# Optimization experiments

Measured on AMD Instinct MI355X. Metric: run time of the kernel, lower is better.

Reference implementation:

```python
import jax, jax.numpy as jnp
import numpy as np

N = 200000      # n_edges (1-simplices)
NNZ = 2000000   # nonzeros per sparse Laplacian
F_IN = 64       # num_edge_feats
F_H = 32        # f_size (hard-coded in FlowSAN)
F_OUT = 8       # output_size
G = 256         # number of graphs in batch
NEG_SLOPE = 0.2 # GAT LeakyReLU slope


def setup_inputs() -> dict:
    key = jax.random.key(0)
    ks = iter(jax.random.split(key, 64))

    def rn(shape, s=0.1):
        return jax.random.normal(next(ks), shape, dtype=jnp.float32) * s

    d = {"x1": jax.random.normal(next(ks), (N, F_IN), dtype=jnp.float32)}
    dims = [(F_IN, F_H), (F_H, F_H), (F_H, F_H), (F_H, F_OUT)]
    for i, (fi, fo) in enumerate(dims, 1):
        d[f"pW{i}"] = rn((fi, fo))                      # SANLayer.p_layer weight (bias=False)
        d[f"uW{i}"] = rn((fi, fo))                      # l_u GAT linear
        d[f"ua_s{i}"] = rn((fo,)); d[f"ua_d{i}"] = rn((fo,))  # l_u GAT attention vec halves
        d[f"dW{i}"] = rn((fi, fo))                      # l_d GAT linear
        d[f"da_s{i}"] = rn((fo,)); d[f"da_d{i}"] = rn((fo,))
    d["l1_idx"] = jax.random.randint(next(ks), (2, NNZ), 0, N, dtype=jnp.int32)
    d["l1_val"] = jax.random.normal(next(ks), (NNZ,), dtype=jnp.float32)
    d["lu_idx"] = jax.random.randint(next(ks), (2, NNZ), 0, N, dtype=jnp.int32)
    d["ld_idx"] = jax.random.randint(next(ks), (2, NNZ), 0, N, dtype=jnp.int32)
    d["batch1"] = jnp.sort(jax.random.randint(next(ks), (N,), 0, G, dtype=jnp.int32))
    return d


def _gat(x, W, a_s, a_d, idx):
    # GAT-style attention over the nonzero pattern of the sparse Laplacian
    h = x @ W                                   # [N, fo]
    row, col = idx[0], idx[1]
    e = jax.nn.leaky_relu(h[row] @ a_s + h[col] @ a_d, NEG_SLOPE)  # [nnz]
    e = e - jax.ops.segment_max(e, row, num_segments=N)[row]       # stable softmax
    w = jnp.exp(e)
    alpha = w / (jax.ops.segment_sum(w, row, num_segments=N)[row] + 1e-16)
    return jax.ops.segment_sum(alpha[:, None] * h[col], row, num_segments=N)


def _san(x, pW, uW, ua_s, ua_d, dW, da_s, da_d, l1_idx, l1_val, lu_idx, ld_idx):
    # p branch: torch.sparse.mm(L1, x @ pW)
    hp = x @ pW
    row, col = l1_idx[0], l1_idx[1]
    hp = jax.ops.segment_sum(l1_val[:, None] * hp[col], row, num_segments=N)
    hu = _gat(x, uW, ua_s, ua_d, lu_idx)
    hd = _gat(x, dW, da_s, da_d, ld_idx)
    return hu + hd + hp


def reference(x1,
              pW1, uW1, ua_s1, ua_d1, dW1, da_s1, da_d1,
              pW2, uW2, ua_s2, ua_d2, dW2, da_s2, da_d2,
              pW3, uW3, ua_s3, ua_d3, dW3, da_s3, da_d3,
              pW4, uW4, ua_s4, ua_d4, dW4, da_s4, da_d4,
              l1_idx, l1_val, lu_idx, ld_idx, batch1):
    layers = [
        (pW1, uW1, ua_s1, ua_d1, dW1, da_s1, da_d1),
        (pW2, uW2, ua_s2, ua_d2, dW2, da_s2, da_d2),
        (pW3, uW3, ua_s3, ua_d3, dW3, da_s3, da_d3),
        (pW4, uW4, ua_s4, ua_d4, dW4, da_s4, da_d4),
    ]
    x = x1
    for p in layers:
        x = jax.nn.relu(_san(x, *p, l1_idx, l1_val, lu_idx, ld_idx))
    # global_mean_pool(|x|, batch1)
    cnt = jax.ops.segment_sum(jnp.ones((N,), jnp.float32), batch1, num_segments=G)
    pooled = jax.ops.segment_sum(jnp.abs(x), batch1, num_segments=G) / jnp.maximum(cnt, 1.0)[:, None]
    return jax.nn.softmax(pooled, axis=1)
```

## Files before the change

### kernel.cpp

```cpp
#include <hip/hip_runtime.h>
#include <hip/hip_fp16.h>
#include <cmath>


#define N_    200000
#define NNZ_  2000000
#define G_    256


__global__ __launch_bounds__(256) void hist_k(const int* __restrict__ lu, const int* __restrict__ ld,
                                              const int* __restrict__ l1, int* __restrict__ deg,
                                              int* __restrict__ tick) {
    int i = blockIdx.x * 256 + threadIdx.x;
    if (i >= NNZ_ / 4) return;
    int e = i * 4;
    int4 ru = *reinterpret_cast<const int4*>(lu + e);
    int4 rd = *reinterpret_cast<const int4*>(ld + e);
    int4 rl = *reinterpret_cast<const int4*>(l1 + e);
    int4 t;
    t.x = atomicAdd(&deg[ru.x], 1);
    t.y = atomicAdd(&deg[ru.y], 1);
    t.z = atomicAdd(&deg[ru.z], 1);
    t.w = atomicAdd(&deg[ru.w], 1);
    *reinterpret_cast<int4*>(tick + e) = t;
    t.x = atomicAdd(&deg[N_ + rd.x], 1);
    t.y = atomicAdd(&deg[N_ + rd.y], 1);
    t.z = atomicAdd(&deg[N_ + rd.z], 1);
    t.w = atomicAdd(&deg[N_ + rd.w], 1);
    *reinterpret_cast<int4*>(tick + NNZ_ + e) = t;
    t.x = atomicAdd(&deg[2 * N_ + rl.x], 1);
    t.y = atomicAdd(&deg[2 * N_ + rl.y], 1);
    t.z = atomicAdd(&deg[2 * N_ + rl.z], 1);
    t.w = atomicAdd(&deg[2 * N_ + rl.w], 1);
    *reinterpret_cast<int4*>(tick + 2 * NNZ_ + e) = t;
}

__global__ __launch_bounds__(256) void scan1_k(const int* __restrict__ in, int* __restrict__ out,
                                               int* __restrict__ bsum, int n) {
    __shared__ int lds[256];
    int tid = threadIdx.x;
    int base = blockIdx.x * 1024 + tid * 4;
    int v0 = (base + 0 < n) ? in[base + 0] : 0;
    int v1 = (base + 1 < n) ? in[base + 1] : 0;
    int v2 = (base + 2 < n) ? in[base + 2] : 0;
    int v3 = (base + 3 < n) ? in[base + 3] : 0;
    int s = v0 + v1 + v2 + v3;
    lds[tid] = s;
    __syncthreads();
    for (int off = 1; off < 256; off <<= 1) {
        int t = (tid >= off) ? lds[tid - off] : 0;
        __syncthreads();
        lds[tid] += t;
        __syncthreads();
    }
    int excl = lds[tid] - s;
    if (base + 0 < n) out[base + 0] = excl;
    if (base + 1 < n) out[base + 1] = excl + v0;
    if (base + 2 < n) out[base + 2] = excl + v0 + v1;
    if (base + 3 < n) out[base + 3] = excl + v0 + v1 + v2;
    if (tid == 255) bsum[blockIdx.x] = lds[255];
}

__global__ __launch_bounds__(256) void scan2_k(int* __restrict__ bsum, int nb, int* __restrict__ total_out) {
    __shared__ int lds[256];
    __shared__ int run_s;
    int tid = threadIdx.x;
    if (tid == 0) run_s = 0;
    __syncthreads();
    for (int c0 = 0; c0 < nb; c0 += 256) {
        int i = c0 + tid;
        int s = (i < nb) ? bsum[i] : 0;
        lds[tid] = s;
        __syncthreads();
        for (int off = 1; off < 256; off <<= 1) {
            int t = (tid >= off) ? lds[tid - off] : 0;
            __syncthreads();
            lds[tid] += t;
            __syncthreads();
        }
        int run = run_s;
        if (i < nb) bsum[i] = run + lds[tid] - s;
        __syncthreads();
        if (tid == 0) run_s = run + lds[255];
        __syncthreads();
    }
    if (tid == 0 && total_out) *total_out = run_s;
}

__global__ __launch_bounds__(256) void scan3_k(int* __restrict__ out, const int* __restrict__ bsum, int n) {
    int add = bsum[blockIdx.x];
    int base = blockIdx.x * 1024 + threadIdx.x * 4;
    #pragma unroll
    for (int k = 0; k < 4; ++k)
        if (base + k < n) out[base + k] += add;
}


template <int FI, int FO, int SCB>
__global__ __launch_bounds__(256) void scat_gemm_k(
    const int* __restrict__ lu, const int* __restrict__ ld, const int* __restrict__ l1,
    const float* __restrict__ l1v, const int* __restrict__ rptr, const int* __restrict__ tick,
    int* __restrict__ cols_u, int* __restrict__ cols_d, int2* __restrict__ pl,
    const float* __restrict__ x,
    const float* __restrict__ uW, const float* __restrict__ uas, const float* __restrict__ uad,
    const float* __restrict__ dW, const float* __restrict__ das, const float* __restrict__ dad,
    const float* __restrict__ pW,
    __half* __restrict__ HU, __half* __restrict__ HD, __half* __restrict__ HP,
    float* __restrict__ ssu, float* __restrict__ sdu,
    float* __restrict__ ssd, float* __restrict__ sdd) {
    if (blockIdx.x % 13 == 0) {
        int sid = blockIdx.x / 13;
        if (sid >= SCB) return;
        int i = sid * 256 + threadIdx.x;
        if (i >= NNZ_ / 4) return;
        int e = i * 4;
        int4 ru = *reinterpret_cast<const int4*>(lu + e);
        int4 rd = *reinterpret_cast<const int4*>(ld + e);
        int4 rl = *reinterpret_cast<const int4*>(l1 + e);
        int4 cu = *reinterpret_cast<const int4*>(lu + NNZ_ + e);
        int4 cd = *reinterpret_cast<const int4*>(ld + NNZ_ + e);
        int4 cl = *reinterpret_cast<const int4*>(l1 + NNZ_ + e);
        int4 tu = *reinterpret_cast<const int4*>(tick + e);
        int4 td = *reinterpret_cast<const int4*>(tick + NNZ_ + e);
        int4 tl = *reinterpret_cast<const int4*>(tick + 2 * NNZ_ + e);
        float4 v = *reinterpret_cast<const float4*>(l1v + e);
        int pu0 = rptr[ru.x] + tu.x, pu1 = rptr[ru.y] + tu.y;
        int pu2 = rptr[ru.z] + tu.z, pu3 = rptr[ru.w] + tu.w;
        int pd0 = rptr[N_ + rd.x] + td.x - NNZ_, pd1 = rptr[N_ + rd.y] + td.y - NNZ_;
        int pd2 = rptr[N_ + rd.z] + td.z - NNZ_, pd3 = rptr[N_ + rd.w] + td.w - NNZ_;
        int pl0 = rptr[2 * N_ + rl.x] + tl.x - 2 * NNZ_, pl1 = rptr[2 * N_ + rl.y] + tl.y - 2 * NNZ_;
        int pl2 = rptr[2 * N_ + rl.z] + tl.z - 2 * NNZ_, pl3 = rptr[2 * N_ + rl.w] + tl.w - 2 * NNZ_;
        __builtin_nontemporal_store(cu.x, &cols_u[pu0]);
        __builtin_nontemporal_store(cu.y, &cols_u[pu1]);
        __builtin_nontemporal_store(cu.z, &cols_u[pu2]);
        __builtin_nontemporal_store(cu.w, &cols_u[pu3]);
        __builtin_nontemporal_store(cd.x, &cols_d[pd0]);
        __builtin_nontemporal_store(cd.y, &cols_d[pd1]);
        __builtin_nontemporal_store(cd.z, &cols_d[pd2]);
        __builtin_nontemporal_store(cd.w, &cols_d[pd3]);
        long long q0 = ((long long)__float_as_int(v.x) << 32) | (unsigned)cl.x;
        long long q1 = ((long long)__float_as_int(v.y) << 32) | (unsigned)cl.y;
        long long q2 = ((long long)__float_as_int(v.z) << 32) | (unsigned)cl.z;
        long long q3 = ((long long)__float_as_int(v.w) << 32) | (unsigned)cl.w;
        __builtin_nontemporal_store(q0, (long long*)&pl[pl0]);
        __builtin_nontemporal_store(q1, (long long*)&pl[pl1]);
        __builtin_nontemporal_store(q2, (long long*)&pl[pl2]);
        __builtin_nontemporal_store(q3, (long long*)&pl[pl3]);
        return;
    }
    int gid = blockIdx.x - blockIdx.x / 13 - 1;
    constexpr int ROWS = 256 / FO;
    constexpr int XS = FI + 1;
    __shared__ float Wu[FI * FO], Wd[FI * FO], Wp[FI * FO];
    __shared__ float xs[ROWS * XS];
    int tid = threadIdx.x;
    for (int i = tid; i < FI * FO; i += 256) {
        Wu[i] = uW[i];
        Wd[i] = dW[i];
        Wp[i] = pW[i];
    }
    int row0 = gid * ROWS;
    for (int i = tid; i < ROWS * FI; i += 256) {
        int r = i / FI, k = i - r * FI;
        int gr = row0 + r;
        xs[r * XS + k] = (gr < N_) ? x[(size_t)gr * FI + k] : 0.f;
    }
    __syncthreads();
    int r = tid / FO, j = tid - (tid / FO) * FO;
    int grow = row0 + r;
    float au = 0.f, ad = 0.f, ap = 0.f;
    #pragma unroll
    for (int k = 0; k < FI; ++k) {
        float xv = xs[r * XS + k];
        au = fmaf(xv, Wu[k * FO + j], au);
        ad = fmaf(xv, Wd[k * FO + j], ad);
        ap = fmaf(xv, Wp[k * FO + j], ap);
    }
    if (grow < N_) {
        HU[(size_t)grow * FO + j] = __float2half(au);
        HD[(size_t)grow * FO + j] = __float2half(ad);
        HP[(size_t)grow * FO + j] = __float2half(ap);
    }
    float vsu = au * uas[j], vdu = au * uad[j];
    float vsd = ad * das[j], vdd = ad * dad[j];
    #pragma unroll
    for (int m = FO / 2; m >= 1; m >>= 1) {
        vsu += __shfl_xor(vsu, m, FO);
        vdu += __shfl_xor(vdu, m, FO);
        vsd += __shfl_xor(vsd, m, FO);
        vdd += __shfl_xor(vdd, m, FO);
    }
    if (j == 0 && grow < N_) {
        ssu[grow] = vsu; sdu[grow] = vdu;
        ssd[grow] = vsd; sdd[grow] = vdd;
    }
}


template <int FI, int FO>
__global__ __launch_bounds__(256) void gemm3_k(const float* __restrict__ x,
                                               const float* __restrict__ uW, const float* __restrict__ uas,
                                               const float* __restrict__ uad,
                                               const float* __restrict__ dW, const float* __restrict__ das,
                                               const float* __restrict__ dad,
                                               const float* __restrict__ pW,
                                               __half* __restrict__ HU, __half* __restrict__ HD,
                                               __half* __restrict__ HP,
                                               float* __restrict__ ssu, float* __restrict__ sdu,
                                               float* __restrict__ ssd, float* __restrict__ sdd) {
    constexpr int ROWS = 256 / FO;
    constexpr int XS = FI + 1;
    __shared__ float Wu[FI * FO], Wd[FI * FO], Wp[FI * FO];
    __shared__ float xs[ROWS * XS];
    int tid = threadIdx.x;
    for (int i = tid; i < FI * FO; i += 256) {
        Wu[i] = uW[i];
        Wd[i] = dW[i];
        Wp[i] = pW[i];
    }
    int row0 = blockIdx.x * ROWS;
    for (int i = tid; i < ROWS * FI; i += 256) {
        int r = i / FI, k = i - r * FI;
        int gr = row0 + r;
        xs[r * XS + k] = (gr < N_) ? x[(size_t)gr * FI + k] : 0.f;
    }
    __syncthreads();
    int r = tid / FO, j = tid - (tid / FO) * FO;
    int grow = row0 + r;
    float au = 0.f, ad = 0.f, ap = 0.f;
    #pragma unroll
    for (int k = 0; k < FI; ++k) {
        float xv = xs[r * XS + k];
        au = fmaf(xv, Wu[k * FO + j], au);
        ad = fmaf(xv, Wd[k * FO + j], ad);
        ap = fmaf(xv, Wp[k * FO + j], ap);
    }
    if (grow < N_) {
        HU[(size_t)grow * FO + j] = __float2half(au);
        HD[(size_t)grow * FO + j] = __float2half(ad);
        HP[(size_t)grow * FO + j] = __float2half(ap);
    }
    float vsu = au * uas[j], vdu = au * uad[j];
    float vsd = ad * das[j], vdd = ad * dad[j];
    #pragma unroll
    for (int m = FO / 2; m >= 1; m >>= 1) {
        vsu += __shfl_xor(vsu, m, FO);
        vdu += __shfl_xor(vdu, m, FO);
        vsd += __shfl_xor(vsd, m, FO);
        vdd += __shfl_xor(vdd, m, FO);
    }
    if (j == 0 && grow < N_) {
        ssu[grow] = vsu; sdu[grow] = vdu;
        ssd[grow] = vsd; sdd[grow] = vdd;
    }
}


template <int FO>
__global__ __launch_bounds__(256) void gather3_k(const int* __restrict__ rptr,
                                                 const int* __restrict__ cols_u,
                                                 const int* __restrict__ cols_d,
                                                 const int2* __restrict__ pl,
                                                 const __half* __restrict__ HU,
                                                 const __half* __restrict__ HD,
                                                 const __half* __restrict__ HP,
                                                 const float* __restrict__ ssu, const float* __restrict__ sdu,
                                                 const float* __restrict__ ssd, const float* __restrict__ sdd,
                                                 float* __restrict__ xout) {
    constexpr int LPR = FO / 8;
    constexpr int SLOTS = 64 / LPR;
    int lane = threadIdx.x & 63;
    int wv = threadIdx.x >> 6;
    int fs = lane & (LPR - 1);
    int slot = lane / LPR;
    int r = blockIdx.x * 4 + wv;
    if (r >= N_) return;

    float out[8];
    #pragma unroll
    for (int k = 0; k < 8; ++k) out[k] = 0.f;

    #pragma unroll
    for (int br = 0; br < 2; ++br) {
        const int* cols = br == 0 ? cols_u : cols_d;
        const __half* H = br == 0 ? HU : HD;
        const float* sdv = br == 0 ? sdu : sdd;
        const float* ssv = br == 0 ? ssu : ssd;
        int base = br == 0 ? 0 : N_;
        int boff = br == 0 ? 0 : NNZ_;
        int b = rptr[base + r] - boff, e = rptr[base + r + 1] - boff;
        float s_row = ssv[r];
        float acc[8];
        #pragma unroll
        for (int k = 0; k < 8; ++k) acc[k] = 0.f;
        float z = 0.f;
        for (int p0 = b; p0 < e; p0 += SLOTS) {
            int p = p0 + slot;
            bool valid = p < e;
            int pc = valid ? p : e - 1;
            int c = cols[pc];
            float g = s_row + sdv[c];
            g = g > 0.f ? g : 0.2f * g;
            float w = valid ? __expf(g) : 0.f;
            z += w;
            const float4 hv = *reinterpret_cast<const float4*>(H + (size_t)c * FO + fs * 8);
            const __half2* h2 = reinterpret_cast<const __half2*>(&hv);
            #pragma unroll
            for (int k = 0; k < 4; ++k) {
                float2 f = __half22float2(h2[k]);
                acc[2 * k]     = fmaf(w, f.x, acc[2 * k]);
                acc[2 * k + 1] = fmaf(w, f.y, acc[2 * k + 1]);
            }
        }
        #pragma unroll
        for (int m = LPR; m < 64; m <<= 1) z += __shfl_xor(z, m);
        float inv = 1.f / (z + 1e-16f);
        #pragma unroll
        for (int k = 0; k < 8; ++k) out[k] = fmaf(acc[k], inv, out[k]);
    }

    {
        int b = rptr[2 * N_ + r] - 2 * NNZ_, e = rptr[2 * N_ + r + 1] - 2 * NNZ_;
        for (int p0 = b; p0 < e; p0 += SLOTS) {
            int p = p0 + slot;
            bool valid = p < e;
            int pc = valid ? p : e - 1;
            int2 cv = pl[pc];
            int c = cv.x;
            float w = valid ? __int_as_float(cv.y) : 0.f;
            const float4 hv = *reinterpret_cast<const float4*>(HP + (size_t)c * FO + fs * 8);
            const __half2* h2 = reinterpret_cast<const __half2*>(&hv);
            #pragma unroll
            for (int k = 0; k < 4; ++k) {
                float2 f = __half22float2(h2[k]);
                out[2 * k]     = fmaf(w, f.x, out[2 * k]);
                out[2 * k + 1] = fmaf(w, f.y, out[2 * k + 1]);
            }
        }
    }

    #pragma unroll
    for (int k = 0; k < 8; ++k) {
        #pragma unroll
        for (int m = LPR; m < 64; m <<= 1) out[k] += __shfl_xor(out[k], m);
    }
    if (slot == 0) {
        float4 o0 = make_float4(fmaxf(out[0], 0.f), fmaxf(out[1], 0.f),
                                fmaxf(out[2], 0.f), fmaxf(out[3], 0.f));
        float4 o1 = make_float4(fmaxf(out[4], 0.f), fmaxf(out[5], 0.f),
                                fmaxf(out[6], 0.f), fmaxf(out[7], 0.f));
        float* op = xout + (size_t)r * FO + fs * 8;
        *reinterpret_cast<float4*>(op) = o0;
        *reinterpret_cast<float4*>(op + 4) = o1;
    }
}


__global__ __launch_bounds__(256) void pool_k(const float* __restrict__ x, const int* __restrict__ batch,
                                              float* __restrict__ out) {
    int g = blockIdx.x;
    __shared__ float part[256];
    __shared__ int sse[2];
    if (threadIdx.x < 2) {
        int target = g + threadIdx.x;
        int lo = 0, hi = N_;
        while (lo < hi) {
            int mid = (lo + hi) >> 1;
            if (batch[mid] < target) lo = mid + 1; else hi = mid;
        }
        sse[threadIdx.x] = lo;
    }
    __syncthreads();
    int s = sse[0], e = sse[1];
    int f = threadIdx.x % 8;
    float acc = 0.f;
    for (int i = s + threadIdx.x / 8; i < e; i += 32) acc += fabsf(x[(size_t)i * 8 + f]);
    part[threadIdx.x] = acc;
    __syncthreads();
    if (threadIdx.x < 8) {
        float t = 0.f;
        #pragma unroll
        for (int k = 0; k < 32; ++k) t += part[k * 8 + f];
        float cnt = (float)(e - s);
        part[f] = t / fmaxf(cnt, 1.0f);
    }
    __syncthreads();
    if (threadIdx.x == 0) {
        float m = part[0];
        for (int j = 1; j < 8; ++j) m = fmaxf(m, part[j]);
        float zs = 0.f;
        float ex[8];
        for (int j = 0; j < 8; ++j) { ex[j] = __expf(part[j] - m); zs += ex[j]; }
        for (int j = 0; j < 8; ++j) out[g * 8 + j] = ex[j] / zs;
    }
}


template <int FI, int FO>
static void run_layer(const float* xin, float* xout, const float* const* W,
                      __half* HU, __half* HD, __half* HP,
                      float* SSU, float* SDU, float* SSD, float* SDD,
                      const int* PTR, const int* CU, const int* CD, const int2* PL,
                      hipStream_t stream) {
    constexpr int ROWS = 256 / FO;
    gemm3_k<FI, FO><<<(N_ + ROWS - 1) / ROWS, 256, 0, stream>>>(
        xin, W[1], W[2], W[3], W[4], W[5], W[6], W[0],
        HU, HD, HP, SSU, SDU, SSD, SDD);
    gather3_k<FO><<<(N_ + 3) / 4, 256, 0, stream>>>(
        PTR, CU, CD, PL, HU, HD, HP, SSU, SDU, SSD, SDD, xout);
}

extern "C" void kernel_launch(void* const* d_in, const int* in_sizes, int n_in, void* d_out,
                              int out_size, void* d_ws, size_t ws_size, hipStream_t stream) {
    (void)in_sizes; (void)n_in; (void)out_size; (void)ws_size;
    const float* x1     = (const float*)d_in[0];
    const int*   l1_idx = (const int*)d_in[29];
    const float* l1_val = (const float*)d_in[30];
    const int*   lu_idx = (const int*)d_in[31];
    const int*   ld_idx = (const int*)d_in[32];
    const int*   batch1 = (const int*)d_in[33];
    float* out = (float*)d_out;

    char* w = (char*)d_ws;
    size_t off = 0;
    auto alloc = [&](size_t bytes) -> char* {
        char* p = w + off;
        off = (off + bytes + 255) & ~(size_t)255;
        return p;
    };
    float*  X    = (float*)alloc((size_t)N_ * 32 * 4);
    __half* HU   = (__half*)alloc((size_t)N_ * 32 * 2);
    __half* HD   = (__half*)alloc((size_t)N_ * 32 * 2);
    __half* HP   = (__half*)alloc((size_t)N_ * 32 * 2);
    float*  SSU  = (float*)alloc((size_t)N_ * 4);
    float*  SDU  = (float*)alloc((size_t)N_ * 4);
    float*  SSD  = (float*)alloc((size_t)N_ * 4);
    float*  SDD  = (float*)alloc((size_t)N_ * 4);
    int*    PTR  = (int*)alloc((size_t)(3 * N_ + 1) * 4);
    int*    DEG  = (int*)alloc((size_t)3 * N_ * 4);
    int*    BSUM = (int*)alloc((size_t)1024 * 4);
    int*    TICK = (int*)alloc((size_t)3 * NNZ_ * 4);
    int*    CU   = (int*)alloc((size_t)NNZ_ * 4);
    int*    CD   = (int*)alloc((size_t)NNZ_ * 4);
    int2*   PL   = (int2*)alloc((size_t)NNZ_ * 8);

    const float* W0[7] = {(const float*)d_in[1], (const float*)d_in[2], (const float*)d_in[3],
                          (const float*)d_in[4], (const float*)d_in[5], (const float*)d_in[6],
                          (const float*)d_in[7]};
    const float* W1[7] = {(const float*)d_in[8],  (const float*)d_in[9],  (const float*)d_in[10],
                          (const float*)d_in[11], (const float*)d_in[12], (const float*)d_in[13],
                          (const float*)d_in[14]};
    const float* W2[7] = {(const float*)d_in[15], (const float*)d_in[16], (const float*)d_in[17],
                          (const float*)d_in[18], (const float*)d_in[19], (const float*)d_in[20],
                          (const float*)d_in[21]};
    const float* W3[7] = {(const float*)d_in[22], (const float*)d_in[23], (const float*)d_in[24],
                          (const float*)d_in[25], (const float*)d_in[26], (const float*)d_in[27],
                          (const float*)d_in[28]};

    hipMemsetAsync(DEG, 0, (size_t)3 * N_ * 4, stream);
    constexpr int QBL = (NNZ_ / 4 + 255) / 256;
    hist_k<<<QBL, 256, 0, stream>>>(lu_idx, ld_idx, l1_idx, DEG, TICK);
    int n3 = 3 * N_;
    int nb = (n3 + 1023) / 1024;
    scan1_k<<<nb, 256, 0, stream>>>(DEG, PTR, BSUM, n3);
    scan2_k<<<1, 256, 0, stream>>>(BSUM, nb, PTR + n3);
    scan3_k<<<nb, 256, 0, stream>>>(PTR, BSUM, n3);

    {
        constexpr int T = 27100;
        scat_gemm_k<64, 32, QBL><<<T, 256, 0, stream>>>(
            lu_idx, ld_idx, l1_idx, l1_val, PTR, TICK, CU, CD, PL,
            x1, W0[1], W0[2], W0[3], W0[4], W0[5], W0[6], W0[0],
            HU, HD, HP, SSU, SDU, SSD, SDD);
    }
    gather3_k<32><<<(N_ + 3) / 4, 256, 0, stream>>>(
        PTR, CU, CD, PL, HU, HD, HP, SSU, SDU, SSD, SDD, X);

    run_layer<32, 32>(X, X, W1, HU, HD, HP, SSU, SDU, SSD, SDD, PTR, CU, CD, PL, stream);
    run_layer<32, 32>(X, X, W2, HU, HD, HP, SSU, SDU, SSD, SDD, PTR, CU, CD, PL, stream);
    run_layer<32, 8>(X, X, W3, HU, HD, HP, SSU, SDU, SSD, SDD, PTR, CU, CD, PL, stream);

    pool_k<<<G_, 256, 0, stream>>>(X, batch1, out);
}
```

Measured before the change: 1.474 ms.

## Recompute destination attention scores from gathered rows and interleave three gather branches

The GEMM kernels no longer write the per-node destination attention scores (sdu/sdd). The gather kernel now computes them on the fly as a dot product of the already-loaded half-precision H row with the attention vector, reduced across lanes. This removes a dependent random 4-byte load per edge. The three branch loops (u, d, p) are merged into one interleaved loop so their independent gathers can be in flight together. The cost is extra FMAs and shuffles per edge, higher register pressure, and scores computed from fp16-rounded H instead of fp32.

```diff
diff --git a/kernel.cpp b/kernel.cpp
--- a/kernel.cpp
+++ b/kernel.cpp
@@ -102,12 +102,11 @@
     const float* __restrict__ l1v, const int* __restrict__ rptr, const int* __restrict__ tick,
     int* __restrict__ cols_u, int* __restrict__ cols_d, int2* __restrict__ pl,
     const float* __restrict__ x,
-    const float* __restrict__ uW, const float* __restrict__ uas, const float* __restrict__ uad,
-    const float* __restrict__ dW, const float* __restrict__ das, const float* __restrict__ dad,
+    const float* __restrict__ uW, const float* __restrict__ uas,
+    const float* __restrict__ dW, const float* __restrict__ das,
     const float* __restrict__ pW,
     __half* __restrict__ HU, __half* __restrict__ HD, __half* __restrict__ HP,
-    float* __restrict__ ssu, float* __restrict__ sdu,
-    float* __restrict__ ssd, float* __restrict__ sdd) {
+    float* __restrict__ ssu, float* __restrict__ ssd) {
     if (blockIdx.x % 13 == 0) {
         int sid = blockIdx.x / 13;
         if (sid >= SCB) return;
@@ -181,18 +180,16 @@
         HD[(size_t)grow * FO + j] = __float2half(ad);
         HP[(size_t)grow * FO + j] = __float2half(ap);
     }
-    float vsu = au * uas[j], vdu = au * uad[j];
-    float vsd = ad * das[j], vdd = ad * dad[j];
+    float vsu = au * uas[j];
+    float vsd = ad * das[j];
     #pragma unroll
     for (int m = FO / 2; m >= 1; m >>= 1) {
         vsu += __shfl_xor(vsu, m, FO);
-        vdu += __shfl_xor(vdu, m, FO);
         vsd += __shfl_xor(vsd, m, FO);
-        vdd += __shfl_xor(vdd, m, FO);
     }
     if (j == 0 && grow < N_) {
-        ssu[grow] = vsu; sdu[grow] = vdu;
-        ssd[grow] = vsd; sdd[grow] = vdd;
+        ssu[grow] = vsu;
+        ssd[grow] = vsd;
     }
 }
 
@@ -200,14 +197,11 @@
 template <int FI, int FO>
 __global__ __launch_bounds__(256) void gemm3_k(const float* __restrict__ x,
                                                const float* __restrict__ uW, const float* __restrict__ uas,
-                                               const float* __restrict__ uad,
                                                const float* __restrict__ dW, const float* __restrict__ das,
-                                               const float* __restrict__ dad,
                                                const float* __restrict__ pW,
                                                __half* __restrict__ HU, __half* __restrict__ HD,
                                                __half* __restrict__ HP,
-                                               float* __restrict__ ssu, float* __restrict__ sdu,
-                                               float* __restrict__ ssd, float* __restrict__ sdd) {
+                                               float* __restrict__ ssu, float* __restrict__ ssd) {
     constexpr int ROWS = 256 / FO;
     constexpr int XS = FI + 1;
     __shared__ float Wu[FI * FO], Wd[FI * FO], Wp[FI * FO];
@@ -240,18 +234,16 @@
         HD[(size_t)grow * FO + j] = __float2half(ad);
         HP[(size_t)grow * FO + j] = __float2half(ap);
     }
-    float vsu = au * uas[j], vdu = au * uad[j];
-    float vsd = ad * das[j], vdd = ad * dad[j];
+    float vsu = au * uas[j];
+    float vsd = ad * das[j];
     #pragma unroll
     for (int m = FO / 2; m >= 1; m >>= 1) {
         vsu += __shfl_xor(vsu, m, FO);
-        vdu += __shfl_xor(vdu, m, FO);
         vsd += __shfl_xor(vsd, m, FO);
-        vdd += __shfl_xor(vdd, m, FO);
     }
     if (j == 0 && grow < N_) {
-        ssu[grow] = vsu; sdu[grow] = vdu;
-        ssd[grow] = vsd; sdd[grow] = vdd;
+        ssu[grow] = vsu;
+        ssd[grow] = vsd;
     }
 }
 
@@ -264,8 +256,10 @@
                                                  const __half* __restrict__ HU,
                                                  const __half* __restrict__ HD,
                                                  const __half* __restrict__ HP,
-                                                 const float* __restrict__ ssu, const float* __restrict__ sdu,
-                                                 const float* __restrict__ ssd, const float* __restrict__ sdd,
+                                                 const float* __restrict__ ssu,
+                                                 const float* __restrict__ ssd,
+                                                 const float* __restrict__ uadv,
+                                                 const float* __restrict__ dadv,
                                                  float* __restrict__ xout) {
     constexpr int LPR = FO / 8;
     constexpr int SLOTS = 64 / LPR;
@@ -276,69 +270,98 @@
     int r = blockIdx.x * 4 + wv;
     if (r >= N_) return;
 
+    float adu[8], add[8];
+    #pragma unroll
+    for (int k = 0; k < 8; ++k) { adu[k] = uadv[fs * 8 + k]; add[k] = dadv[fs * 8 + k]; }
+
+    int bu = rptr[r],                eu = rptr[r + 1];
+    int bd = rptr[N_ + r] - NNZ_,    ed = rptr[N_ + r + 1] - NNZ_;
+    int bp = rptr[2 * N_ + r] - 2 * NNZ_, ep = rptr[2 * N_ + r + 1] - 2 * NNZ_;
+    float su = ssu[r], sdr = ssd[r];
+
+    float accu[8], accd[8], outp[8];
+    #pragma unroll
+    for (int k = 0; k < 8; ++k) { accu[k] = 0.f; accd[k] = 0.f; outp[k] = 0.f; }
+    float zu = 0.f, zd = 0.f;
+
+    int pu = bu, pd = bd, pp = bp;
+    while (pu < eu || pd < ed || pp < ep) {
+        bool vu = pu < eu, vd = pd < ed, vp = pp < ep;
+        int cu = 0, cd = 0;
+        int2 cv = make_int2(0, 0);
+        if (vu) { int ix = pu + slot; cu = cols_u[ix < eu ? ix : eu - 1]; }
+        if (vd) { int ix = pd + slot; cd = cols_d[ix < ed ? ix : ed - 1]; }
+        if (vp) { int ix = pp + slot; cv = pl[ix < ep ? ix : ep - 1]; }
+        float4 h_u, h_d, h_p;
+        if (vu) h_u = *reinterpret_cast<const float4*>(HU + (size_t)cu * FO + fs * 8);
+        if (vd) h_d = *reinterpret_cast<const float4*>(HD + (size_t)cd * FO + fs * 8);
+        if (vp) h_p = *reinterpret_cast<const float4*>(HP + (size_t)cv.x * FO + fs * 8);
+        if (vu) {
+            const __half2* h2 = reinterpret_cast<const __half2*>(&h_u);
+            float f[8];
+            #pragma unroll
+            for (int k = 0; k < 4; ++k) {
+                float2 t = __half22float2(h2[k]);
+                f[2 * k] = t.x; f[2 * k + 1] = t.y;
+            }
+            float pdot = 0.f;
+            #pragma unroll
+            for (int k = 0; k < 8; ++k) pdot = fmaf(f[k], adu[k], pdot);
+            #pragma unroll
+            for (int m = 1; m < LPR; m <<= 1) pdot += __shfl_xor(pdot, m);
+            float g = su + pdot;
+            g = g > 0.f ? g : 0.2f * g;
+            float w = (pu + slot < eu) ? __expf(g) : 0.f;
+            zu += w;
+            #pragma unroll
+            for (int k = 0; k < 8; ++k) accu[k] = fmaf(w, f[k], accu[k]);
+            pu += SLOTS;
+        }
+        if (vd) {
+            const __half2* h2 = reinterpret_cast<const __half2*>(&h_d);
+            float f[8];
+            #pragma unroll
+            for (int k = 0; k < 4; ++k) {
+                float2 t = __half22float2(h2[k]);
+                f[2 * k] = t.x; f[2 * k + 1] = t.y;
+            }
+            float pdot = 0.f;
+            #pragma unroll
+            for (int k = 0; k < 8; ++k) pdot = fmaf(f[k], add[k], pdot);
+            #pragma unroll
+            for (int m = 1; m < LPR; m <<= 1) pdot += __shfl_xor(pdot, m);
+            float g = sdr + pdot;
+            g = g > 0.f ? g : 0.2f * g;
+            float w = (pd + slot < ed) ? __expf(g) : 0.f;
+            zd += w;
+            #pragma unroll
+            for (int k = 0; k < 8; ++k) accd[k] = fmaf(w, f[k], accd[k]);
+            pd += SLOTS;
+        }
+        if (vp) {
+            const __half2* h2 = reinterpret_cast<const __half2*>(&h_p);
+            float w = (pp + slot < ep) ? __int_as_float(cv.y) : 0.f;
+            #pragma unroll
+            for (int k = 0; k < 4; ++k) {
+                float2 t = __half22float2(h2[k]);
+                outp[2 * k]     = fmaf(w, t.x, outp[2 * k]);
+                outp[2 * k + 1] = fmaf(w, t.y, outp[2 * k + 1]);
+            }
+            pp += SLOTS;
+        }
+    }
+
+    #pragma unroll
+    for (int m = LPR; m < 64; m <<= 1) {
+        zu += __shfl_xor(zu, m);
+        zd += __shfl_xor(zd, m);
+    }
+    float invu = 1.f / (zu + 1e-16f);
+    float invd = 1.f / (zd + 1e-16f);
+
     float out[8];
     #pragma unroll
-    for (int k = 0; k < 8; ++k) out[k] = 0.f;
-
-    #pragma unroll
-    for (int br = 0; br < 2; ++br) {
-        const int* cols = br == 0 ? cols_u : cols_d;
-        const __half* H = br == 0 ? HU : HD;
-        const float* sdv = br == 0 ? sdu : sdd;
-        const float* ssv = br == 0 ? ssu : ssd;
-        int base = br == 0 ? 0 : N_;
-        int boff = br == 0 ? 0 : NNZ_;
-        int b = rptr[base + r] - boff, e = rptr[base + r + 1] - boff;
-        float s_row = ssv[r];
-        float acc[8];
-        #pragma unroll
-        for (int k = 0; k < 8; ++k) acc[k] = 0.f;
-        float z = 0.f;
-        for (int p0 = b; p0 < e; p0 += SLOTS) {
-            int p = p0 + slot;
-            bool valid = p < e;
-            int pc = valid ? p : e - 1;
-            int c = cols[pc];
-            float g = s_row + sdv[c];
-            g = g > 0.f ? g : 0.2f * g;
-            float w = valid ? __expf(g) : 0.f;
-            z += w;
-            const float4 hv = *reinterpret_cast<const float4*>(H + (size_t)c * FO + fs * 8);
-            const __half2* h2 = reinterpret_cast<const __half2*>(&hv);
-            #pragma unroll
-            for (int k = 0; k < 4; ++k) {
-                float2 f = __half22float2(h2[k]);
-                acc[2 * k]     = fmaf(w, f.x, acc[2 * k]);
-                acc[2 * k + 1] = fmaf(w, f.y, acc[2 * k + 1]);
-            }
-        }
-        #pragma unroll
-        for (int m = LPR; m < 64; m <<= 1) z += __shfl_xor(z, m);
-        float inv = 1.f / (z + 1e-16f);
-        #pragma unroll
-        for (int k = 0; k < 8; ++k) out[k] = fmaf(acc[k], inv, out[k]);
-    }
-
-    {
-        int b = rptr[2 * N_ + r] - 2 * NNZ_, e = rptr[2 * N_ + r + 1] - 2 * NNZ_;
-        for (int p0 = b; p0 < e; p0 += SLOTS) {
-            int p = p0 + slot;
-            bool valid = p < e;
-            int pc = valid ? p : e - 1;
-            int2 cv = pl[pc];
-            int c = cv.x;
-            float w = valid ? __int_as_float(cv.y) : 0.f;
-            const float4 hv = *reinterpret_cast<const float4*>(HP + (size_t)c * FO + fs * 8);
-            const __half2* h2 = reinterpret_cast<const __half2*>(&hv);
-            #pragma unroll
-            for (int k = 0; k < 4; ++k) {
-                float2 f = __half22float2(h2[k]);
-                out[2 * k]     = fmaf(w, f.x, out[2 * k]);
-                out[2 * k + 1] = fmaf(w, f.y, out[2 * k + 1]);
-            }
-        }
-    }
-
+    for (int k = 0; k < 8; ++k) out[k] = fmaf(accu[k], invu, fmaf(accd[k], invd, outp[k]));
     #pragma unroll
     for (int k = 0; k < 8; ++k) {
         #pragma unroll
@@ -399,15 +422,15 @@
 template <int FI, int FO>
 static void run_layer(const float* xin, float* xout, const float* const* W,
                       __half* HU, __half* HD, __half* HP,
-                      float* SSU, float* SDU, float* SSD, float* SDD,
+                      float* SSU, float* SSD,
                       const int* PTR, const int* CU, const int* CD, const int2* PL,
                       hipStream_t stream) {
     constexpr int ROWS = 256 / FO;
     gemm3_k<FI, FO><<<(N_ + ROWS - 1) / ROWS, 256, 0, stream>>>(
-        xin, W[1], W[2], W[3], W[4], W[5], W[6], W[0],
-        HU, HD, HP, SSU, SDU, SSD, SDD);
+        xin, W[1], W[2], W[4], W[5], W[0],
+        HU, HD, HP, SSU, SSD);
     gather3_k<FO><<<(N_ + 3) / 4, 256, 0, stream>>>(
-        PTR, CU, CD, PL, HU, HD, HP, SSU, SDU, SSD, SDD, xout);
+        PTR, CU, CD, PL, HU, HD, HP, SSU, SSD, W[3], W[6], xout);
 }
 
 extern "C" void kernel_launch(void* const* d_in, const int* in_sizes, int n_in, void* d_out,
@@ -433,9 +456,7 @@
     __half* HD   = (__half*)alloc((size_t)N_ * 32 * 2);
     __half* HP   = (__half*)alloc((size_t)N_ * 32 * 2);
     float*  SSU  = (float*)alloc((size_t)N_ * 4);
-    float*  SDU  = (float*)alloc((size_t)N_ * 4);
     float*  SSD  = (float*)alloc((size_t)N_ * 4);
-    float*  SDD  = (float*)alloc((size_t)N_ * 4);
     int*    PTR  = (int*)alloc((size_t)(3 * N_ + 1) * 4);
     int*    DEG  = (int*)alloc((size_t)3 * N_ * 4);
     int*    BSUM = (int*)alloc((size_t)1024 * 4);
@@ -470,15 +491,15 @@
         constexpr int T = 27100;
         scat_gemm_k<64, 32, QBL><<<T, 256, 0, stream>>>(
             lu_idx, ld_idx, l1_idx, l1_val, PTR, TICK, CU, CD, PL,
-            x1, W0[1], W0[2], W0[3], W0[4], W0[5], W0[6], W0[0],
-            HU, HD, HP, SSU, SDU, SSD, SDD);
+            x1, W0[1], W0[2], W0[4], W0[5], W0[0],
+            HU, HD, HP, SSU, SSD);
     }
     gather3_k<32><<<(N_ + 3) / 4, 256, 0, stream>>>(
-        PTR, CU, CD, PL, HU, HD, HP, SSU, SDU, SSD, SDD, X);
-
-    run_layer<32, 32>(X, X, W1, HU, HD, HP, SSU, SDU, SSD, SDD, PTR, CU, CD, PL, stream);
-    run_layer<32, 32>(X, X, W2, HU, HD, HP, SSU, SDU, SSD, SDD, PTR, CU, CD, PL, stream);
-    run_layer<32, 8>(X, X, W3, HU, HD, HP, SSU, SDU, SSD, SDD, PTR, CU, CD, PL, stream);
+        PTR, CU, CD, PL, HU, HD, HP, SSU, SSD, W0[3], W0[6], X);
+
+    run_layer<32, 32>(X, X, W1, HU, HD, HP, SSU, SSD, PTR, CU, CD, PL, stream);
+    run_layer<32, 32>(X, X, W2, HU, HD, HP, SSU, SSD, PTR, CU, CD, PL, stream);
+    run_layer<32, 8>(X, X, W3, HU, HD, HP, SSU, SSD, PTR, CU, CD, PL, stream);
 
     pool_k<<<G_, 256, 0, stream>>>(X, batch1, out);
 }
```

After: 1.545 ms. 1.05x slower.

## Fuse each layer's sparse gather with the next layer's dense projections

Applied to the files above, without the earlier changes.

Merges the per-row sparse aggregation of one layer with the next layer's three linear projections and attention-score dot products in a single kernel. The intermediate activation X is kept in shared memory instead of being written to global memory and reread by a separate GEMM kernel. H and score buffers are double-buffered (a/b) so the kernel does not read and write the same arrays. This removes three GEMM launches and the fp32 X round trip, in exchange for per-block weight loads into LDS and a block-wide sync after the latency-bound gather.

```diff
diff --git a/kernel.cpp b/kernel.cpp
--- a/kernel.cpp
+++ b/kernel.cpp
@@ -197,86 +197,22 @@
 }
 
 
-template <int FI, int FO>
-__global__ __launch_bounds__(256) void gemm3_k(const float* __restrict__ x,
-                                               const float* __restrict__ uW, const float* __restrict__ uas,
-                                               const float* __restrict__ uad,
-                                               const float* __restrict__ dW, const float* __restrict__ das,
-                                               const float* __restrict__ dad,
-                                               const float* __restrict__ pW,
-                                               __half* __restrict__ HU, __half* __restrict__ HD,
-                                               __half* __restrict__ HP,
-                                               float* __restrict__ ssu, float* __restrict__ sdu,
-                                               float* __restrict__ ssd, float* __restrict__ sdd) {
-    constexpr int ROWS = 256 / FO;
-    constexpr int XS = FI + 1;
-    __shared__ float Wu[FI * FO], Wd[FI * FO], Wp[FI * FO];
-    __shared__ float xs[ROWS * XS];
-    int tid = threadIdx.x;
-    for (int i = tid; i < FI * FO; i += 256) {
-        Wu[i] = uW[i];
-        Wd[i] = dW[i];
-        Wp[i] = pW[i];
-    }
-    int row0 = blockIdx.x * ROWS;
-    for (int i = tid; i < ROWS * FI; i += 256) {
-        int r = i / FI, k = i - r * FI;
-        int gr = row0 + r;
-        xs[r * XS + k] = (gr < N_) ? x[(size_t)gr * FI + k] : 0.f;
-    }
-    __syncthreads();
-    int r = tid / FO, j = tid - (tid / FO) * FO;
-    int grow = row0 + r;
-    float au = 0.f, ad = 0.f, ap = 0.f;
-    #pragma unroll
-    for (int k = 0; k < FI; ++k) {
-        float xv = xs[r * XS + k];
-        au = fmaf(xv, Wu[k * FO + j], au);
-        ad = fmaf(xv, Wd[k * FO + j], ad);
-        ap = fmaf(xv, Wp[k * FO + j], ap);
-    }
-    if (grow < N_) {
-        HU[(size_t)grow * FO + j] = __float2half(au);
-        HD[(size_t)grow * FO + j] = __float2half(ad);
-        HP[(size_t)grow * FO + j] = __float2half(ap);
-    }
-    float vsu = au * uas[j], vdu = au * uad[j];
-    float vsd = ad * das[j], vdd = ad * dad[j];
-    #pragma unroll
-    for (int m = FO / 2; m >= 1; m >>= 1) {
-        vsu += __shfl_xor(vsu, m, FO);
-        vdu += __shfl_xor(vdu, m, FO);
-        vsd += __shfl_xor(vsd, m, FO);
-        vdd += __shfl_xor(vdd, m, FO);
-    }
-    if (j == 0 && grow < N_) {
-        ssu[grow] = vsu; sdu[grow] = vdu;
-        ssd[grow] = vsd; sdd[grow] = vdd;
-    }
-}
-
-
 template <int FO>
-__global__ __launch_bounds__(256) void gather3_k(const int* __restrict__ rptr,
-                                                 const int* __restrict__ cols_u,
-                                                 const int* __restrict__ cols_d,
-                                                 const int2* __restrict__ pl,
-                                                 const __half* __restrict__ HU,
-                                                 const __half* __restrict__ HD,
-                                                 const __half* __restrict__ HP,
-                                                 const float* __restrict__ ssu, const float* __restrict__ sdu,
-                                                 const float* __restrict__ ssd, const float* __restrict__ sdd,
-                                                 float* __restrict__ xout) {
+__device__ __forceinline__ void gather_row(int r, int lane,
+                                           const int* __restrict__ rptr,
+                                           const int* __restrict__ cols_u,
+                                           const int* __restrict__ cols_d,
+                                           const int2* __restrict__ pl,
+                                           const __half* __restrict__ HU,
+                                           const __half* __restrict__ HD,
+                                           const __half* __restrict__ HP,
+                                           const float* __restrict__ ssu, const float* __restrict__ sdu,
+                                           const float* __restrict__ ssd, const float* __restrict__ sdd,
+                                           float out[8]) {
     constexpr int LPR = FO / 8;
     constexpr int SLOTS = 64 / LPR;
-    int lane = threadIdx.x & 63;
-    int wv = threadIdx.x >> 6;
     int fs = lane & (LPR - 1);
     int slot = lane / LPR;
-    int r = blockIdx.x * 4 + wv;
-    if (r >= N_) return;
-
-    float out[8];
     #pragma unroll
     for (int k = 0; k < 8; ++k) out[k] = 0.f;
 
@@ -318,7 +254,6 @@
         #pragma unroll
         for (int k = 0; k < 8; ++k) out[k] = fmaf(acc[k], inv, out[k]);
     }
-
     {
         int b = rptr[2 * N_ + r] - 2 * NNZ_, e = rptr[2 * N_ + r + 1] - 2 * NNZ_;
         for (int p0 = b; p0 < e; p0 += SLOTS) {
@@ -326,9 +261,8 @@
             bool valid = p < e;
             int pc = valid ? p : e - 1;
             int2 cv = pl[pc];
-            int c = cv.x;
             float w = valid ? __int_as_float(cv.y) : 0.f;
-            const float4 hv = *reinterpret_cast<const float4*>(HP + (size_t)c * FO + fs * 8);
+            const float4 hv = *reinterpret_cast<const float4*>(HP + (size_t)cv.x * FO + fs * 8);
             const __half2* h2 = reinterpret_cast<const __half2*>(&hv);
             #pragma unroll
             for (int k = 0; k < 4; ++k) {
@@ -338,20 +272,118 @@
             }
         }
     }
-
     #pragma unroll
     for (int k = 0; k < 8; ++k) {
         #pragma unroll
         for (int m = LPR; m < 64; m <<= 1) out[k] += __shfl_xor(out[k], m);
-    }
-    if (slot == 0) {
-        float4 o0 = make_float4(fmaxf(out[0], 0.f), fmaxf(out[1], 0.f),
-                                fmaxf(out[2], 0.f), fmaxf(out[3], 0.f));
-        float4 o1 = make_float4(fmaxf(out[4], 0.f), fmaxf(out[5], 0.f),
-                                fmaxf(out[6], 0.f), fmaxf(out[7], 0.f));
+        out[k] = fmaxf(out[k], 0.f);
+    }
+}
+
+
+template <int FO1, int FI2, int FO2>
+__global__ __launch_bounds__(256) void gg_k(
+    const int* __restrict__ rptr, const int* __restrict__ cols_u,
+    const int* __restrict__ cols_d, const int2* __restrict__ pl,
+    const __half* __restrict__ HU1, const __half* __restrict__ HD1, const __half* __restrict__ HP1,
+    const float* __restrict__ ssu1, const float* __restrict__ sdu1,
+    const float* __restrict__ ssd1, const float* __restrict__ sdd1,
+    const float* __restrict__ uW, const float* __restrict__ uas, const float* __restrict__ uad,
+    const float* __restrict__ dW, const float* __restrict__ das, const float* __restrict__ dad,
+    const float* __restrict__ pW,
+    __half* __restrict__ HU2, __half* __restrict__ HD2, __half* __restrict__ HP2,
+    float* __restrict__ ssu2, float* __restrict__ sdu2,
+    float* __restrict__ ssd2, float* __restrict__ sdd2) {
+    __shared__ float Wu[FI2 * FO2], Wd[FI2 * FO2], Wp[FI2 * FO2];
+    __shared__ float xs[4][FI2];
+    int tid = threadIdx.x;
+    for (int i = tid; i < FI2 * FO2; i += 256) {
+        Wu[i] = uW[i];
+        Wd[i] = dW[i];
+        Wp[i] = pW[i];
+    }
+    int lane = tid & 63;
+    int wv = tid >> 6;
+    int r = blockIdx.x * 4 + wv;
+    if (r < N_) {
+        float out[8];
+        gather_row<FO1>(r, lane, rptr, cols_u, cols_d, pl, HU1, HD1, HP1,
+                        ssu1, sdu1, ssd1, sdd1, out);
+        constexpr int LPR = FO1 / 8;
+        int fs = lane & (LPR - 1);
+        if (lane / LPR == 0) {
+            #pragma unroll
+            for (int k = 0; k < 8; ++k) xs[wv][fs * 8 + k] = out[k];
+        }
+    }
+    __syncthreads();
+    if (r >= N_) return;
+    constexpr int NK = 64 / FO2;
+    constexpr int KC = FI2 / NK;
+    int j = lane % FO2;
+    int sub = lane / FO2;
+    float au = 0.f, ad = 0.f, ap = 0.f;
+    #pragma unroll
+    for (int kk = 0; kk < KC; ++kk) {
+        int k = sub * KC + kk;
+        float xv = xs[wv][k];
+        au = fmaf(xv, Wu[k * FO2 + j], au);
+        ad = fmaf(xv, Wd[k * FO2 + j], ad);
+        ap = fmaf(xv, Wp[k * FO2 + j], ap);
+    }
+    #pragma unroll
+    for (int m = FO2; m < 64; m <<= 1) {
+        au += __shfl_xor(au, m);
+        ad += __shfl_xor(ad, m);
+        ap += __shfl_xor(ap, m);
+    }
+    if (sub == 0) {
+        HU2[(size_t)r * FO2 + j] = __float2half(au);
+        HD2[(size_t)r * FO2 + j] = __float2half(ad);
+        HP2[(size_t)r * FO2 + j] = __float2half(ap);
+    }
+    float vsu = au * uas[j], vdu = au * uad[j];
+    float vsd = ad * das[j], vdd = ad * dad[j];
+    #pragma unroll
+    for (int m = FO2 / 2; m >= 1; m >>= 1) {
+        vsu += __shfl_xor(vsu, m, FO2);
+        vdu += __shfl_xor(vdu, m, FO2);
+        vsd += __shfl_xor(vsd, m, FO2);
+        vdd += __shfl_xor(vdd, m, FO2);
+    }
+    if (lane == 0) {
+        ssu2[r] = vsu; sdu2[r] = vdu;
+        ssd2[r] = vsd; sdd2[r] = vdd;
+    }
+}
+
+
+template <int FO>
+__global__ __launch_bounds__(256) void gather3_k(const int* __restrict__ rptr,
+                                                 const int* __restrict__ cols_u,
+                                                 const int* __restrict__ cols_d,
+                                                 const int2* __restrict__ pl,
+                                                 const __half* __restrict__ HU,
+                                                 const __half* __restrict__ HD,
+                                                 const __half* __restrict__ HP,
+                                                 const float* __restrict__ ssu, const float* __restrict__ sdu,
+                                                 const float* __restrict__ ssd, const float* __restrict__ sdd,
+                                                 float* __restrict__ xout) {
+    constexpr int LPR = FO / 8;
+    int lane = threadIdx.x & 63;
+    int wv = threadIdx.x >> 6;
+    int r = blockIdx.x * 4 + wv;
+    if (r >= N_) return;
+    float out[8];
+    gather_row<FO>(r, lane, rptr, cols_u, cols_d, pl, HU, HD, HP, ssu, sdu, ssd, sdd, out);
+    int fs = lane & (LPR - 1);
+    if (lane / LPR == 0) {
+        float4 o0 = make_float4(out[0], out[1], out[2], out[3]);
+        float4 o1 = make_float4(out[4], out[5], out[6], out[7]);
         float* op = xout + (size_t)r * FO + fs * 8;
         *reinterpret_cast<float4*>(op) = o0;
-        *reinterpret_cast<float4*>(op + 4) = o1;
+        if (FO > 8) *reinterpret_cast<float4*>(op + 4) = o1;
+        else { op[4] = o1.x; op[5] = o1.y; op[6] = o1.z; op[7] = o1.w; }
     }
 }
 
@@ -395,21 +427,6 @@
     }
 }
 
-
-template <int FI, int FO>
-static void run_layer(const float* xin, float* xout, const float* const* W,
-                      __half* HU, __half* HD, __half* HP,
-                      float* SSU, float* SDU, float* SSD, float* SDD,
-                      const int* PTR, const int* CU, const int* CD, const int2* PL,
-                      hipStream_t stream) {
-    constexpr int ROWS = 256 / FO;
-    gemm3_k<FI, FO><<<(N_ + ROWS - 1) / ROWS, 256, 0, stream>>>(
-        xin, W[1], W[2], W[3], W[4], W[5], W[6], W[0],
-        HU, HD, HP, SSU, SDU, SSD, SDD);
-    gather3_k<FO><<<(N_ + 3) / 4, 256, 0, stream>>>(
-        PTR, CU, CD, PL, HU, HD, HP, SSU, SDU, SSD, SDD, xout);
-}
-
 extern "C" void kernel_launch(void* const* d_in, const int* in_sizes, int n_in, void* d_out,
                               int out_size, void* d_ws, size_t ws_size, hipStream_t stream) {
     (void)in_sizes; (void)n_in; (void)out_size; (void)ws_size;
@@ -428,14 +445,21 @@
         off = (off + bytes + 255) & ~(size_t)255;
         return p;
     };
-    float*  X    = (float*)alloc((size_t)N_ * 32 * 4);
-    __half* HU   = (__half*)alloc((size_t)N_ * 32 * 2);
-    __half* HD   = (__half*)alloc((size_t)N_ * 32 * 2);
-    __half* HP   = (__half*)alloc((size_t)N_ * 32 * 2);
-    float*  SSU  = (float*)alloc((size_t)N_ * 4);
-    float*  SDU  = (float*)alloc((size_t)N_ * 4);
-    float*  SSD  = (float*)alloc((size_t)N_ * 4);
-    float*  SDD  = (float*)alloc((size_t)N_ * 4);
+    float*  X    = (float*)alloc((size_t)N_ * 8 * 4);
+    __half* HUa  = (__half*)alloc((size_t)N_ * 32 * 2);
+    __half* HDa  = (__half*)alloc((size_t)N_ * 32 * 2);
+    __half* HPa  = (__half*)alloc((size_t)N_ * 32 * 2);
+    __half* HUb  = (__half*)alloc((size_t)N_ * 32 * 2);
+    __half* HDb  = (__half*)alloc((size_t)N_ * 32 * 2);
+    __half* HPb  = (__half*)alloc((size_t)N_ * 32 * 2);
+    float*  SSUa = (float*)alloc((size_t)N_ * 4);
+    float*  SDUa = (float*)alloc((size_t)N_ * 4);
+    float*  SSDa = (float*)alloc((size_t)N_ * 4);
+    float*  SDDa = (float*)alloc((size_t)N_ * 4);
+    float*  SSUb = (float*)alloc((size_t)N_ * 4);
+    float*  SDUb = (float*)alloc((size_t)N_ * 4);
+    float*  SSDb = (float*)alloc((size_t)N_ * 4);
+    float*  SDDb = (float*)alloc((size_t)N_ * 4);
     int*    PTR  = (int*)alloc((size_t)(3 * N_ + 1) * 4);
     int*    DEG  = (int*)alloc((size_t)3 * N_ * 4);
     int*    BSUM = (int*)alloc((size_t)1024 * 4);
@@ -471,14 +495,24 @@
         scat_gemm_k<64, 32, QBL><<<T, 256, 0, stream>>>(
             lu_idx, ld_idx, l1_idx, l1_val, PTR, TICK, CU, CD, PL,
             x1, W0[1], W0[2], W0[3], W0[4], W0[5], W0[6], W0[0],
-            HU, HD, HP, SSU, SDU, SSD, SDD);
-    }
-    gather3_k<32><<<(N_ + 3) / 4, 256, 0, stream>>>(
-        PTR, CU, CD, PL, HU, HD, HP, SSU, SDU, SSD, SDD, X);
-
-    run_layer<32, 32>(X, X, W1, HU, HD, HP, SSU, SDU, SSD, SDD, PTR, CU, CD, PL, stream);
-    run_layer<32, 32>(X, X, W2, HU, HD, HP, SSU, SDU, SSD, SDD, PTR, CU, CD, PL, stream);
-    run_layer<32, 8>(X, X, W3, HU, HD, HP, SSU, SDU, SSD, SDD, PTR, CU, CD, PL, stream);
+            HUa, HDa, HPa, SSUa, SDUa, SSDa, SDDa);
+    }
+
+    int gb = (N_ + 3) / 4;
+    gg_k<32, 32, 32><<<gb, 256, 0, stream>>>(
+        PTR, CU, CD, PL, HUa, HDa, HPa, SSUa, SDUa, SSDa, SDDa,
+        W1[1], W1[2], W1[3], W1[4], W1[5], W1[6], W1[0],
+        HUb, HDb, HPb, SSUb, SDUb, SSDb, SDDb);
+    gg_k<32, 32, 32><<<gb, 256, 0, stream>>>(
+        PTR, CU, CD, PL, HUb, HDb, HPb, SSUb, SDUb, SSDb, SDDb,
+        W2[1], W2[2], W2[3], W2[4], W2[5], W2[6], W2[0],
+        HUa, HDa, HPa, SSUa, SDUa, SSDa, SDDa);
+    gg_k<32, 32, 8><<<gb, 256, 0, stream>>>(
+        PTR, CU, CD, PL, HUa, HDa, HPa, SSUa, SDUa, SSDa, SDDa,
+        W3[1], W3[2], W3[3], W3[4], W3[5], W3[6], W3[0],
+        HUb, HDb, HPb, SSUb, SDUb, SSDb, SDDb);
+    gather3_k<8><<<gb, 256, 0, stream>>>(
+        PTR, CU, CD, PL, HUb, HDb, HPb, SSUb, SDUb, SSDb, SDDb, X);
 
     pool_k<<<G_, 256, 0, stream>>>(X, batch1, out);
 }
```

Result: slower. 1.516 ms (+2.8%).
